# Performance work log

Measured on AMD Instinct MI355X. Metric: run time of the kernel, lower is better.

## Reference

```python
import jax, jax.numpy as jnp
import numpy as np
import math

D_MODEL = 1024
N_HEAD = 16
D_K = D_MODEL // N_HEAD
NEG_INF = -1e30  # fp32 mask fill value used by the torch module


def _rope(x, b_rotate=None):
    # x: [b, h, n, k], k even. Interleaved (even/odd) RoPE, matching the torch code.
    b, h, n, k = x.shape
    half = k // 2
    inv_freq = 1.0 / (10000.0 ** (jnp.arange(half, dtype=jnp.float32) / half))  # [half]
    ang = jnp.arange(n, dtype=jnp.float32)[:, None] * inv_freq[None, :]          # [n, half]
    sin = jnp.sin(ang)
    cos = jnp.cos(ang)
    x1 = x[..., 0::2]  # [b,h,n,half]
    x2 = x[..., 1::2]
    even = x1 * cos - x2 * sin
    odd = x1 * sin + x2 * cos
    out = jnp.stack([even, odd], axis=-1).reshape(b, h, n, k)  # re-interleave
    if b_rotate is not None:
        out = out * b_rotate  # barope multiplicative term
    return out


def setup_inputs() -> dict:
    key = jax.random.key(0)
    ks = jax.random.split(key, 7)
    B, S = 1, 2048
    query = jax.random.normal(ks[0], (B, S, D_MODEL), dtype=jnp.float32)
    kk = jax.random.normal(ks[1], (B, S, D_MODEL), dtype=jnp.float32)
    value = jax.random.normal(ks[2], (B, S, D_MODEL), dtype=jnp.float32)
    b_emb = jax.random.normal(ks[3], (B, S, D_MODEL), dtype=jnp.float32)
    mask = jax.random.bernoulli(ks[4], 0.9, (B, S))  # bool [B,S]
    linear_layers = 0.02 * jax.random.normal(ks[5], (3, D_MODEL, N_HEAD, D_K), dtype=jnp.float32)
    b_proj = jax.random.normal(ks[6], (D_MODEL, N_HEAD, D_K), dtype=jnp.float32)
    return {"query": query, "key": kk, "value": value, "b_emb": b_emb,
            "mask": mask, "linear_layers": linear_layers, "b_proj": b_proj}


def reference(query, key, value, b_emb, mask, linear_layers, b_proj):
    B, S, _ = query.shape
    # QKV projections: [b,n,d] x [d,h,k] -> [b,h,n,k]
    q = jnp.einsum('bnd,dhk->bhnk', query, linear_layers[0])
    k = jnp.einsum('bnd,dhk->bhnk', key, linear_layers[1])
    v = jnp.einsum('bnd,dhk->bhnk', value, linear_layers[2])
    # barope=True branch: multiplicative rotation modifier from b_emb
    b_rotate = jnp.einsum('bnd,dhk->bhnk', b_emb, b_proj)
    q = _rope(q, b_rotate)
    k = _rope(k, b_rotate)
    scores = jnp.einsum('bhqk,bhmk->bhqm', q, k) / math.sqrt(D_K)  # [b,h,s,s]
    pair_mask = (mask[:, :, None] & mask[:, None, :])[:, None]     # [b,1,s,s]
    scores = jnp.where(pair_mask, scores, NEG_INF)
    p_attn = jax.nn.softmax(scores, axis=-1)  # dropout p=0 -> identity
    x = jnp.einsum('bhqm,bhmk->bhqk', p_attn, v)
    return x.transpose(0, 2, 1, 3).reshape(B, S, N_HEAD * D_K)
```

## Files before the change

kernel.cpp:

```cpp
#include <hip/hip_runtime.h>
#include <hip/hip_bf16.h>
#include <math.h>

#define S_LEN 2048
#define NHEAD 16
#define DMODEL 1024

typedef short bf16x8 __attribute__((ext_vector_type(8)));
typedef float f32x4 __attribute__((ext_vector_type(4)));

static __device__ __forceinline__ unsigned short bfbits(float x) {
    __hip_bfloat16 h = __float2bfloat16(x);
    unsigned short u; __builtin_memcpy(&u, &h, 2); return u;
}
static __device__ __forceinline__ float bf2f(unsigned short u) {
    union { unsigned int i; float f; } v; v.i = ((unsigned int)u) << 16; return v.f;
}
static __device__ __forceinline__ void splitRN(float x, unsigned short& hi, unsigned short& lo) {
    unsigned short h = bfbits(x);
    float r = x - bf2f(h);
    hi = h; lo = bfbits(r);
}
static __device__ __forceinline__ void split4(float4 x, ushort4& h4, ushort4& l4) {
    unsigned short h0,l0,h1,l1,h2,l2,h3,l3;
    splitRN(x.x,h0,l0); splitRN(x.y,h1,l1); splitRN(x.z,h2,l2); splitRN(x.w,h3,l3);
    h4 = make_ushort4(h0,h1,h2,h3); l4 = make_ushort4(l0,l1,l2,l3);
}

__device__ __forceinline__ int mask_at(const void* mp, int enc, int s) {
    if (enc) return ((const unsigned char*)mp)[s] != 0;
    return ((const unsigned int*)mp)[s] != 0u;
}

__global__ void detect_kernel(const void* __restrict__ mask, int* __restrict__ flags) {
    if (threadIdx.x == 0 && blockIdx.x == 0) {
        const unsigned int* m = (const unsigned int*)mask;
        int bytey = 0;
        for (int i = 0; i < 8; ++i) {
            unsigned int u = m[i];
            if (u != 0u && u != 1u && u != 0x3F800000u) bytey = 1;
        }
        flags[0] = bytey;
    }
}

__global__ __launch_bounds__(256)
void presplit_w(const float* __restrict__ ll, const float* __restrict__ bproj,
                unsigned short* __restrict__ Wh, unsigned short* __restrict__ Wl) {
    __shared__ unsigned short Th[64][72], Tl[64][72];
    const int t = threadIdx.x;
    const int bid = blockIdx.x;
    const int stream = bid >> 8;
    const int rem = bid & 255;
    const int h = rem >> 4;
    const int d0 = (rem & 15) << 6;
    const float* src = (stream == 3) ? bproj : (ll + (size_t)stream * 1048576);
#pragma unroll
    for (int rep = 0; rep < 4; ++rep) {
        int fid = rep * 256 + t;
        int dl = fid >> 4, n4 = (fid & 15) * 4;
        float4 w = *(const float4*)&src[(size_t)(d0 + dl) * 1024 + h * 64 + n4];
        unsigned short hh, lo2;
#pragma unroll
        for (int m = 0; m < 4; ++m) { splitRN((&w.x)[m], hh, lo2); Th[n4+m][dl] = hh; Tl[n4+m][dl] = lo2; }
    }
    __syncthreads();
    size_t obase = (size_t)stream * 1048576;
#pragma unroll
    for (int rep = 0; rep < 2; ++rep) {
        int wid = rep * 256 + t;
        int n = wid >> 3, dl8 = (wid & 7) * 8;
        int dtile = n >> 4, cc = n & 15;
        int dglob = d0 + dl8;
        int kc = dglob >> 5;
        int qd = (dglob >> 3) & 3;
        size_t off = obase + (size_t)(h * 4 + dtile) * 16384 + (size_t)kc * 512
                   + (size_t)(qd * 16 + cc) * 8;
        *(uint4*)&Wh[off] = *(uint4*)&Th[n][dl8];
        *(uint4*)&Wl[off] = *(uint4*)&Tl[n][dl8];
    }
}

__global__ __launch_bounds__(256, 4)
void proj_fused5(const float* __restrict__ Xq, const float* __restrict__ Xk,
                 const float* __restrict__ Xv, const float* __restrict__ Xb,
                 const unsigned short* __restrict__ Wh, const unsigned short* __restrict__ Wl,
                 unsigned short* __restrict__ qhi, unsigned short* __restrict__ qlo,
                 unsigned short* __restrict__ khi, unsigned short* __restrict__ klo,
                 unsigned short* __restrict__ vhi) {
    __shared__ unsigned short smem[8960];
    unsigned short (*XQh)[40] = (unsigned short(*)[40])(smem + 0 * 1280);
    unsigned short (*XQl)[40] = (unsigned short(*)[40])(smem + 1 * 1280);
    unsigned short (*XKh)[40] = (unsigned short(*)[40])(smem + 2 * 1280);
    unsigned short (*XKl)[40] = (unsigned short(*)[40])(smem + 3 * 1280);
    unsigned short (*XVh)[40] = (unsigned short(*)[40])(smem + 4 * 1280);
    unsigned short (*XBh)[40] = (unsigned short(*)[40])(smem + 5 * 1280);
    unsigned short (*XBl)[40] = (unsigned short(*)[40])(smem + 6 * 1280);
    unsigned short (*T0)[72] = (unsigned short(*)[72])(smem + 0);
    unsigned short (*T1)[72] = (unsigned short(*)[72])(smem + 2304);
    unsigned short (*T2)[40] = (unsigned short(*)[40])(smem + 4608);

    const int t = threadIdx.x;
    const int lin = blockIdx.x;
    const int xcd = lin & 7;
    const int inner = lin >> 3;
    const int h = inner >> 3;
    const int sg = inner & 7;
    const int s0 = (xcd * 8 + sg) * 32;
    const int lane = t & 63, dt = t >> 6, quad = lane >> 4, c = lane & 15;

    f32x4 aq[2], ak[2], av[2], ab[2];
#pragma unroll
    for (int i = 0; i < 2; ++i) {
        aq[i] = (f32x4){0.f,0.f,0.f,0.f}; ak[i] = (f32x4){0.f,0.f,0.f,0.f};
        av[i] = (f32x4){0.f,0.f,0.f,0.f}; ab[i] = (f32x4){0.f,0.f,0.f,0.f};
    }

    const int xr = t >> 3, xc = (t & 7) * 4;
    const size_t xg = (size_t)(s0 + xr) * DMODEL + xc;
    const size_t wb = (size_t)(h * 4 + dt) * 16384 + (size_t)lane * 8;

    float4 pq, pk, pv, pb;
    pq = *(const float4*)&Xq[xg];
    pk = *(const float4*)&Xk[xg];
    pv = *(const float4*)&Xv[xg];
    pb = *(const float4*)&Xb[xg];

    for (int kc = 0; kc < 32; ++kc) {
        __syncthreads();
        {
            ushort4 h4, l4;
            split4(pq, h4, l4); *(ushort4*)&XQh[xr][xc] = h4; *(ushort4*)&XQl[xr][xc] = l4;
            split4(pk, h4, l4); *(ushort4*)&XKh[xr][xc] = h4; *(ushort4*)&XKl[xr][xc] = l4;
            split4(pb, h4, l4); *(ushort4*)&XBh[xr][xc] = h4; *(ushort4*)&XBl[xr][xc] = l4;
            *(ushort4*)&XVh[xr][xc] = make_ushort4(bfbits(pv.x),bfbits(pv.y),bfbits(pv.z),bfbits(pv.w));
        }
        __syncthreads();

        size_t wo = wb + (size_t)kc * 512;
        bf16x8 aQh = *(const bf16x8*)&Wh[wo];
        bf16x8 aQl = *(const bf16x8*)&Wl[wo];
        bf16x8 aKh = *(const bf16x8*)&Wh[1048576 + wo];
        bf16x8 aKl = *(const bf16x8*)&Wl[1048576 + wo];
        bf16x8 aVh = *(const bf16x8*)&Wh[2097152 + wo];
        bf16x8 aVl = *(const bf16x8*)&Wl[2097152 + wo];
        bf16x8 aBh = *(const bf16x8*)&Wh[3145728 + wo];
        bf16x8 aBl = *(const bf16x8*)&Wl[3145728 + wo];

        if (kc + 1 < 32) {
            size_t g = xg + (size_t)(kc + 1) * 32;
            pq = *(const float4*)&Xq[g];
            pk = *(const float4*)&Xk[g];
            pv = *(const float4*)&Xv[g];
            pb = *(const float4*)&Xb[g];
        }

#pragma unroll
        for (int st = 0; st < 2; ++st) {
            bf16x8 b1 = *(bf16x8*)&XQh[st*16+c][quad*8];
            bf16x8 b2 = *(bf16x8*)&XQl[st*16+c][quad*8];
            aq[st] = __builtin_amdgcn_mfma_f32_16x16x32_bf16(aQh, b1, aq[st], 0, 0, 0);
            aq[st] = __builtin_amdgcn_mfma_f32_16x16x32_bf16(aQh, b2, aq[st], 0, 0, 0);
            aq[st] = __builtin_amdgcn_mfma_f32_16x16x32_bf16(aQl, b1, aq[st], 0, 0, 0);
            aq[st] = __builtin_amdgcn_mfma_f32_16x16x32_bf16(aQl, b2, aq[st], 0, 0, 0);
            b1 = *(bf16x8*)&XKh[st*16+c][quad*8];
            b2 = *(bf16x8*)&XKl[st*16+c][quad*8];
            ak[st] = __builtin_amdgcn_mfma_f32_16x16x32_bf16(aKh, b1, ak[st], 0, 0, 0);
            ak[st] = __builtin_amdgcn_mfma_f32_16x16x32_bf16(aKh, b2, ak[st], 0, 0, 0);
            ak[st] = __builtin_amdgcn_mfma_f32_16x16x32_bf16(aKl, b1, ak[st], 0, 0, 0);
            ak[st] = __builtin_amdgcn_mfma_f32_16x16x32_bf16(aKl, b2, ak[st], 0, 0, 0);
            b1 = *(bf16x8*)&XVh[st*16+c][quad*8];
            av[st] = __builtin_amdgcn_mfma_f32_16x16x32_bf16(aVh, b1, av[st], 0, 0, 0);
            av[st] = __builtin_amdgcn_mfma_f32_16x16x32_bf16(aVl, b1, av[st], 0, 0, 0);
            b1 = *(bf16x8*)&XBh[st*16+c][quad*8];
            b2 = *(bf16x8*)&XBl[st*16+c][quad*8];
            ab[st] = __builtin_amdgcn_mfma_f32_16x16x32_bf16(aBh, b1, ab[st], 0, 0, 0);
            ab[st] = __builtin_amdgcn_mfma_f32_16x16x32_bf16(aBh, b2, ab[st], 0, 0, 0);
            ab[st] = __builtin_amdgcn_mfma_f32_16x16x32_bf16(aBl, b1, ab[st], 0, 0, 0);
            ab[st] = __builtin_amdgcn_mfma_f32_16x16x32_bf16(aBl, b2, ab[st], 0, 0, 0);
        }
    }

    float rq[2][4], rk[2][4];
    {
        int p0 = dt * 8 + 2 * quad;
        double inv0 = pow(10000.0, -(double)p0 / 32.0);
        double inv1 = pow(10000.0, -(double)(p0 + 1) / 32.0);
#pragma unroll
        for (int st = 0; st < 2; ++st) {
            int s = s0 + st * 16 + c;
            double a0 = (double)s * inv0, a1 = (double)s * inv1;
            float sn0 = (float)sin(a0), cs0 = (float)cos(a0);
            float sn1 = (float)sin(a1), cs1 = (float)cos(a1);
            rq[st][0] = (aq[st][0]*cs0 - aq[st][1]*sn0) * ab[st][0];
            rq[st][1] = (aq[st][0]*sn0 + aq[st][1]*cs0) * ab[st][1];
            rq[st][2] = (aq[st][2]*cs1 - aq[st][3]*sn1) * ab[st][2];
            rq[st][3] = (aq[st][2]*sn1 + aq[st][3]*cs1) * ab[st][3];
            rk[st][0] = (ak[st][0]*cs0 - ak[st][1]*sn0) * ab[st][0];
            rk[st][1] = (ak[st][0]*sn0 + ak[st][1]*cs0) * ab[st][1];
            rk[st][2] = (ak[st][2]*cs1 - ak[st][3]*sn1) * ab[st][2];
            rk[st][3] = (ak[st][2]*sn1 + ak[st][3]*cs1) * ab[st][3];
        }
    }
    __syncthreads();
#pragma unroll
    for (int st = 0; st < 2; ++st) {
        unsigned short h0,l0,h1,l1,h2,l2,h3,l3;
        splitRN(rq[st][0],h0,l0); splitRN(rq[st][1],h1,l1);
        splitRN(rq[st][2],h2,l2); splitRN(rq[st][3],h3,l3);
        *(ushort4*)&T0[st*16+c][dt*16+4*quad] = make_ushort4(h0,h1,h2,h3);
        *(ushort4*)&T1[st*16+c][dt*16+4*quad] = make_ushort4(l0,l1,l2,l3);
#pragma unroll
        for (int reg = 0; reg < 4; ++reg)
            T2[dt * 16 + 4 * quad + reg][st * 16 + c] = bfbits(av[st][reg]);
    }
    __syncthreads();
    {
        int row = t >> 3, d8 = (t & 7) * 8;
        size_t qb = ((size_t)(h * S_LEN + s0 + row)) * 64 + d8;
        *(uint4*)&qhi[qb] = *(uint4*)&T0[row][d8];
        *(uint4*)&qlo[qb] = *(uint4*)&T1[row][d8];
        int d = t >> 2, s8 = (t & 3) * 8;
        size_t vb = ((size_t)(h * 64 + d)) * S_LEN + s0 + s8;
        *(uint4*)&vhi[vb] = *(uint4*)&T2[d][s8];
    }
    __syncthreads();
#pragma unroll
    for (int st = 0; st < 2; ++st) {
        unsigned short h0,l0,h1,l1,h2,l2,h3,l3;
        splitRN(rk[st][0],h0,l0); splitRN(rk[st][1],h1,l1);
        splitRN(rk[st][2],h2,l2); splitRN(rk[st][3],h3,l3);
        *(ushort4*)&T0[st*16+c][dt*16+4*quad] = make_ushort4(h0,h1,h2,h3);
        *(ushort4*)&T1[st*16+c][dt*16+4*quad] = make_ushort4(l0,l1,l2,l3);
    }
    __syncthreads();
    {
        int row = t >> 3, d8 = (t & 7) * 8;
        size_t qb = ((size_t)(h * S_LEN + s0 + row)) * 64 + d8;
        *(uint4*)&khi[qb] = *(uint4*)&T0[row][d8];
        *(uint4*)&klo[qb] = *(uint4*)&T1[row][d8];
    }
}

__global__ __launch_bounds__(256)
void attn_mfma(const unsigned short* __restrict__ qh, const unsigned short* __restrict__ ql,
               const unsigned short* __restrict__ kh, const unsigned short* __restrict__ kl,
               const unsigned short* __restrict__ vh,
               const void* __restrict__ mask, float* __restrict__ out,
               const int* __restrict__ flags) {
    __shared__ unsigned short Kh[2][64][72], Kl[2][64][72];
    __shared__ unsigned short Vt[2][64][72];
    __shared__ unsigned short Sh[64][72], Sl[64][72];
    const int menc = flags[0];
    const int t = threadIdx.x;
    const int lin = blockIdx.x + (blockIdx.y << 5);
    const int h = (lin & 7) * 2 + ((lin >> 3) & 1);
    const int s0 = (lin >> 4) * 64;
    const int lane = t & 63, w = t >> 6, quad = lane >> 4, c = lane & 15;

    bf16x8 qfh[2], qfl[2];
#pragma unroll
    for (int ks = 0; ks < 2; ++ks) {
        size_t base = ((size_t)(h * S_LEN + s0 + 16 * w + c)) * 64 + ks * 32 + quad * 8;
        qfh[ks] = *(const bf16x8*)&qh[base];
        qfl[ks] = *(const bf16x8*)&ql[base];
    }
    int mq[4];
#pragma unroll
    for (int i = 0; i < 4; ++i) mq[i] = mask_at(mask, menc, s0 + 16 * w + quad * 4 + i);

    float m_i[4], l_i[4];
#pragma unroll
    for (int i = 0; i < 4; ++i) { m_i[i] = -INFINITY; l_i[i] = 0.0f; }
    f32x4 o_acc[4];
#pragma unroll
    for (int i = 0; i < 4; ++i) o_acc[i] = (f32x4){0.f,0.f,0.f,0.f};

    uint4 pre[6];
#pragma unroll
    for (int i = 0; i < 2; ++i) {
        int id = i * 256 + t, row = id >> 3, col8 = (id & 7) * 8;
        size_t kb = ((size_t)(h * S_LEN + row)) * 64 + col8;
        size_t vb = ((size_t)(h * 64 + row)) * S_LEN + col8;
        pre[0 + i] = *(const uint4*)&kh[kb];
        pre[2 + i] = *(const uint4*)&kl[kb];
        pre[4 + i] = *(const uint4*)&vh[vb];
    }
#pragma unroll
    for (int i = 0; i < 2; ++i) {
        int id = i * 256 + t, row = id >> 3, col8 = (id & 7) * 8;
        *(uint4*)&Kh[0][row][col8] = pre[0 + i];
        *(uint4*)&Kl[0][row][col8] = pre[2 + i];
        *(uint4*)&Vt[0][row][col8] = pre[4 + i];
    }
    __syncthreads();

    int cur = 0;
    for (int kt = 0; kt < 32; ++kt) {
        if (kt + 1 < 32) {
            const int kb0 = (kt + 1) * 64;
#pragma unroll
            for (int i = 0; i < 2; ++i) {
                int id = i * 256 + t, row = id >> 3, col8 = (id & 7) * 8;
                size_t kb = ((size_t)(h * S_LEN + kb0 + row)) * 64 + col8;
                size_t vb = ((size_t)(h * 64 + row)) * S_LEN + kb0 + col8;
                pre[0 + i] = *(const uint4*)&kh[kb];
                pre[2 + i] = *(const uint4*)&kl[kb];
                pre[4 + i] = *(const uint4*)&vh[vb];
            }
        }
        int mk[4];
#pragma unroll
        for (int nt = 0; nt < 4; ++nt) mk[nt] = mask_at(mask, menc, kt * 64 + 16 * nt + c);

        f32x4 sc[4];
#pragma unroll
        for (int i = 0; i < 4; ++i) sc[i] = (f32x4){0.f,0.f,0.f,0.f};
#pragma unroll
        for (int nt = 0; nt < 4; ++nt)
#pragma unroll
            for (int ks = 0; ks < 2; ++ks) {
                bf16x8 kfh = *(bf16x8*)&Kh[cur][nt * 16 + c][ks * 32 + quad * 8];
                bf16x8 kfl = *(bf16x8*)&Kl[cur][nt * 16 + c][ks * 32 + quad * 8];
                sc[nt] = __builtin_amdgcn_mfma_f32_16x16x32_bf16(qfh[ks], kfh, sc[nt], 0, 0, 0);
                sc[nt] = __builtin_amdgcn_mfma_f32_16x16x32_bf16(qfh[ks], kfl, sc[nt], 0, 0, 0);
                sc[nt] = __builtin_amdgcn_mfma_f32_16x16x32_bf16(qfl[ks], kfh, sc[nt], 0, 0, 0);
            }

        float sm[4][4];
#pragma unroll
        for (int nt = 0; nt < 4; ++nt)
#pragma unroll
            for (int reg = 0; reg < 4; ++reg)
                sm[nt][reg] = (mq[reg] && mk[nt]) ? sc[nt][reg] * 0.125f : -1e30f;

        float rmax[4];
#pragma unroll
        for (int reg = 0; reg < 4; ++reg)
            rmax[reg] = fmaxf(fmaxf(sm[0][reg], sm[1][reg]), fmaxf(sm[2][reg], sm[3][reg]));
#pragma unroll
        for (int off = 1; off <= 8; off <<= 1)
#pragma unroll
            for (int reg = 0; reg < 4; ++reg)
                rmax[reg] = fmaxf(rmax[reg], __shfl_xor(rmax[reg], off, 64));

        float mn[4], alpha[4];
#pragma unroll
        for (int reg = 0; reg < 4; ++reg) {
            mn[reg] = fmaxf(m_i[reg], rmax[reg]);
            alpha[reg] = __expf(m_i[reg] - mn[reg]);
            m_i[reg] = mn[reg];
        }

        float rsum[4] = {0.f, 0.f, 0.f, 0.f};
#pragma unroll
        for (int nt = 0; nt < 4; ++nt)
#pragma unroll
            for (int reg = 0; reg < 4; ++reg) {
                float e = __expf(sm[nt][reg] - mn[reg]);
                rsum[reg] += e;
                unsigned short eh, el;
                splitRN(e, eh, el);
                Sh[16 * w + quad * 4 + reg][16 * nt + c] = eh;
                Sl[16 * w + quad * 4 + reg][16 * nt + c] = el;
            }
#pragma unroll
        for (int off = 1; off <= 8; off <<= 1)
#pragma unroll
            for (int reg = 0; reg < 4; ++reg)
                rsum[reg] += __shfl_xor(rsum[reg], off, 64);
#pragma unroll
        for (int reg = 0; reg < 4; ++reg) l_i[reg] = l_i[reg] * alpha[reg] + rsum[reg];
        if (!__all(alpha[0] == 1.0f && alpha[1] == 1.0f &&
                   alpha[2] == 1.0f && alpha[3] == 1.0f)) {
#pragma unroll
            for (int nt = 0; nt < 4; ++nt)
#pragma unroll
                for (int reg = 0; reg < 4; ++reg) o_acc[nt][reg] *= alpha[reg];
        }

        if (kt + 1 < 32) {
            const int nxt = cur ^ 1;
#pragma unroll
            for (int i = 0; i < 2; ++i) {
                int id = i * 256 + t, row = id >> 3, col8 = (id & 7) * 8;
                *(uint4*)&Kh[nxt][row][col8] = pre[0 + i];
                *(uint4*)&Kl[nxt][row][col8] = pre[2 + i];
                *(uint4*)&Vt[nxt][row][col8] = pre[4 + i];
            }
        }

#pragma unroll
        for (int ks = 0; ks < 2; ++ks) {
            bf16x8 pfh = *(bf16x8*)&Sh[16 * w + c][ks * 32 + quad * 8];
            bf16x8 pfl = *(bf16x8*)&Sl[16 * w + c][ks * 32 + quad * 8];
#pragma unroll
            for (int nt = 0; nt < 4; ++nt) {
                bf16x8 vf = *(bf16x8*)&Vt[cur][nt * 16 + c][ks * 32 + quad * 8];
                o_acc[nt] = __builtin_amdgcn_mfma_f32_16x16x32_bf16(pfh, vf, o_acc[nt], 0, 0, 0);
                o_acc[nt] = __builtin_amdgcn_mfma_f32_16x16x32_bf16(pfl, vf, o_acc[nt], 0, 0, 0);
            }
        }
        __syncthreads();
        cur ^= 1;
    }

#pragma unroll
    for (int reg = 0; reg < 4; ++reg) {
        float inv = 1.0f / l_i[reg];
        int row = s0 + 16 * w + quad * 4 + reg;
#pragma unroll
        for (int nt = 0; nt < 4; ++nt)
            out[(size_t)row * 1024 + h * 64 + nt * 16 + c] = o_acc[nt][reg] * inv;
    }
}

extern "C" void kernel_launch(void* const* d_in, const int* in_sizes, int n_in,
                              void* d_out, int out_size, void* d_ws, size_t ws_size,
                              hipStream_t stream) {
    const float* query = (const float*)d_in[0];
    const float* key   = (const float*)d_in[1];
    const float* value = (const float*)d_in[2];
    const float* b_emb = (const float*)d_in[3];
    const void*  mask  = d_in[4];
    const float* ll    = (const float*)d_in[5];
    const float* bproj = (const float*)d_in[6];
    float* out = (float*)d_out;

    const size_t HSD = (size_t)NHEAD * S_LEN * 64;
    char* ws = (char*)d_ws;
    int* flags = (int*)ws;
    unsigned short* qhi = (unsigned short*)(ws + 4096);
    unsigned short* qlo = qhi + HSD;
    unsigned short* khi = qlo + HSD;
    unsigned short* klo = khi + HSD;
    unsigned short* vhi = klo + HSD;
    unsigned short* Wh  = vhi + HSD;
    unsigned short* Wl  = Wh + 4 * 1048576;

    dim3 pb(256);
    detect_kernel<<<1, 64, 0, stream>>>(mask, flags);
    presplit_w<<<1024, pb, 0, stream>>>(ll, bproj, Wh, Wl);
    proj_fused5<<<1024, pb, 0, stream>>>(query, key, value, b_emb,
                                         Wh, Wl, qhi, qlo, khi, klo, vhi);
    attn_mfma<<<dim3(32, 16), pb, 0, stream>>>(qhi, qlo, khi, klo, vhi, mask, out, flags);
}
```

Before: 268.8 us.

## Double-buffer projection LDS tiles and shrink attention blocks to two waves

The projection kernel now double-buffers its split activation tiles in LDS. It writes the next chunk while MFMAs consume the current one, which cuts the per-iteration barriers from two to one, at the cost of doubling LDS. The attention kernel moves to 128-thread blocks covering 32 query rows, giving 1024 blocks. It drops its K/V LDS double buffer in favour of register prefetch plus a single buffer with two barriers per tile. The aim is more blocks and occupancy for attention, but each block now loads K/V for fewer query rows, so global traffic per output roughly doubles.

```diff
diff --git a/kernel.cpp b/kernel.cpp
--- a/kernel.cpp
+++ b/kernel.cpp
@@ -82,20 +82,13 @@
 }
 
 __global__ __launch_bounds__(256, 4)
-void proj_fused5(const float* __restrict__ Xq, const float* __restrict__ Xk,
+void proj_fused6(const float* __restrict__ Xq, const float* __restrict__ Xk,
                  const float* __restrict__ Xv, const float* __restrict__ Xb,
                  const unsigned short* __restrict__ Wh, const unsigned short* __restrict__ Wl,
                  unsigned short* __restrict__ qhi, unsigned short* __restrict__ qlo,
                  unsigned short* __restrict__ khi, unsigned short* __restrict__ klo,
                  unsigned short* __restrict__ vhi) {
-    __shared__ unsigned short smem[8960];
-    unsigned short (*XQh)[40] = (unsigned short(*)[40])(smem + 0 * 1280);
-    unsigned short (*XQl)[40] = (unsigned short(*)[40])(smem + 1 * 1280);
-    unsigned short (*XKh)[40] = (unsigned short(*)[40])(smem + 2 * 1280);
-    unsigned short (*XKl)[40] = (unsigned short(*)[40])(smem + 3 * 1280);
-    unsigned short (*XVh)[40] = (unsigned short(*)[40])(smem + 4 * 1280);
-    unsigned short (*XBh)[40] = (unsigned short(*)[40])(smem + 5 * 1280);
-    unsigned short (*XBl)[40] = (unsigned short(*)[40])(smem + 6 * 1280);
+    __shared__ unsigned short smem[17920];
     unsigned short (*T0)[72] = (unsigned short(*)[72])(smem + 0);
     unsigned short (*T1)[72] = (unsigned short(*)[72])(smem + 2304);
     unsigned short (*T2)[40] = (unsigned short(*)[40])(smem + 4608);
@@ -120,23 +113,30 @@
     const size_t xg = (size_t)(s0 + xr) * DMODEL + xc;
     const size_t wb = (size_t)(h * 4 + dt) * 16384 + (size_t)lane * 8;
 
+#define XARR(name, b, i) unsigned short (*name)[40] = (unsigned short(*)[40])(smem + (b) * 8960 + (i) * 1280)
+
     float4 pq, pk, pv, pb;
     pq = *(const float4*)&Xq[xg];
     pk = *(const float4*)&Xk[xg];
     pv = *(const float4*)&Xv[xg];
     pb = *(const float4*)&Xb[xg];
+    {
+        XARR(XQh,0,0); XARR(XQl,0,1); XARR(XKh,0,2); XARR(XKl,0,3);
+        XARR(XVh,0,4); XARR(XBh,0,5); XARR(XBl,0,6);
+        ushort4 h4, l4;
+        split4(pq, h4, l4); *(ushort4*)&XQh[xr][xc] = h4; *(ushort4*)&XQl[xr][xc] = l4;
+        split4(pk, h4, l4); *(ushort4*)&XKh[xr][xc] = h4; *(ushort4*)&XKl[xr][xc] = l4;
+        split4(pb, h4, l4); *(ushort4*)&XBh[xr][xc] = h4; *(ushort4*)&XBl[xr][xc] = l4;
+        *(ushort4*)&XVh[xr][xc] = make_ushort4(bfbits(pv.x),bfbits(pv.y),bfbits(pv.z),bfbits(pv.w));
+    }
+    pq = *(const float4*)&Xq[xg + 32];
+    pk = *(const float4*)&Xk[xg + 32];
+    pv = *(const float4*)&Xv[xg + 32];
+    pb = *(const float4*)&Xb[xg + 32];
+    __syncthreads();
 
     for (int kc = 0; kc < 32; ++kc) {
-        __syncthreads();
-        {
-            ushort4 h4, l4;
-            split4(pq, h4, l4); *(ushort4*)&XQh[xr][xc] = h4; *(ushort4*)&XQl[xr][xc] = l4;
-            split4(pk, h4, l4); *(ushort4*)&XKh[xr][xc] = h4; *(ushort4*)&XKl[xr][xc] = l4;
-            split4(pb, h4, l4); *(ushort4*)&XBh[xr][xc] = h4; *(ushort4*)&XBl[xr][xc] = l4;
-            *(ushort4*)&XVh[xr][xc] = make_ushort4(bfbits(pv.x),bfbits(pv.y),bfbits(pv.z),bfbits(pv.w));
-        }
-        __syncthreads();
-
+        const int cb = kc & 1, nb = cb ^ 1;
         size_t wo = wb + (size_t)kc * 512;
         bf16x8 aQh = *(const bf16x8*)&Wh[wo];
         bf16x8 aQl = *(const bf16x8*)&Wl[wo];
@@ -148,38 +148,53 @@
         bf16x8 aBl = *(const bf16x8*)&Wl[3145728 + wo];
 
         if (kc + 1 < 32) {
-            size_t g = xg + (size_t)(kc + 1) * 32;
+            XARR(XQh,nb,0); XARR(XQl,nb,1); XARR(XKh,nb,2); XARR(XKl,nb,3);
+            XARR(XVh,nb,4); XARR(XBh,nb,5); XARR(XBl,nb,6);
+            ushort4 h4, l4;
+            split4(pq, h4, l4); *(ushort4*)&XQh[xr][xc] = h4; *(ushort4*)&XQl[xr][xc] = l4;
+            split4(pk, h4, l4); *(ushort4*)&XKh[xr][xc] = h4; *(ushort4*)&XKl[xr][xc] = l4;
+            split4(pb, h4, l4); *(ushort4*)&XBh[xr][xc] = h4; *(ushort4*)&XBl[xr][xc] = l4;
+            *(ushort4*)&XVh[xr][xc] = make_ushort4(bfbits(pv.x),bfbits(pv.y),bfbits(pv.z),bfbits(pv.w));
+        }
+        if (kc + 2 < 32) {
+            size_t g = xg + (size_t)(kc + 2) * 32;
             pq = *(const float4*)&Xq[g];
             pk = *(const float4*)&Xk[g];
             pv = *(const float4*)&Xv[g];
             pb = *(const float4*)&Xb[g];
         }
 
-#pragma unroll
-        for (int st = 0; st < 2; ++st) {
-            bf16x8 b1 = *(bf16x8*)&XQh[st*16+c][quad*8];
-            bf16x8 b2 = *(bf16x8*)&XQl[st*16+c][quad*8];
-            aq[st] = __builtin_amdgcn_mfma_f32_16x16x32_bf16(aQh, b1, aq[st], 0, 0, 0);
-            aq[st] = __builtin_amdgcn_mfma_f32_16x16x32_bf16(aQh, b2, aq[st], 0, 0, 0);
-            aq[st] = __builtin_amdgcn_mfma_f32_16x16x32_bf16(aQl, b1, aq[st], 0, 0, 0);
-            aq[st] = __builtin_amdgcn_mfma_f32_16x16x32_bf16(aQl, b2, aq[st], 0, 0, 0);
-            b1 = *(bf16x8*)&XKh[st*16+c][quad*8];
-            b2 = *(bf16x8*)&XKl[st*16+c][quad*8];
-            ak[st] = __builtin_amdgcn_mfma_f32_16x16x32_bf16(aKh, b1, ak[st], 0, 0, 0);
-            ak[st] = __builtin_amdgcn_mfma_f32_16x16x32_bf16(aKh, b2, ak[st], 0, 0, 0);
-            ak[st] = __builtin_amdgcn_mfma_f32_16x16x32_bf16(aKl, b1, ak[st], 0, 0, 0);
-            ak[st] = __builtin_amdgcn_mfma_f32_16x16x32_bf16(aKl, b2, ak[st], 0, 0, 0);
-            b1 = *(bf16x8*)&XVh[st*16+c][quad*8];
-            av[st] = __builtin_amdgcn_mfma_f32_16x16x32_bf16(aVh, b1, av[st], 0, 0, 0);
-            av[st] = __builtin_amdgcn_mfma_f32_16x16x32_bf16(aVl, b1, av[st], 0, 0, 0);
-            b1 = *(bf16x8*)&XBh[st*16+c][quad*8];
-            b2 = *(bf16x8*)&XBl[st*16+c][quad*8];
-            ab[st] = __builtin_amdgcn_mfma_f32_16x16x32_bf16(aBh, b1, ab[st], 0, 0, 0);
-            ab[st] = __builtin_amdgcn_mfma_f32_16x16x32_bf16(aBh, b2, ab[st], 0, 0, 0);
-            ab[st] = __builtin_amdgcn_mfma_f32_16x16x32_bf16(aBl, b1, ab[st], 0, 0, 0);
-            ab[st] = __builtin_amdgcn_mfma_f32_16x16x32_bf16(aBl, b2, ab[st], 0, 0, 0);
-        }
-    }
+        {
+            XARR(XQh,cb,0); XARR(XQl,cb,1); XARR(XKh,cb,2); XARR(XKl,cb,3);
+            XARR(XVh,cb,4); XARR(XBh,cb,5); XARR(XBl,cb,6);
+#pragma unroll
+            for (int st = 0; st < 2; ++st) {
+                bf16x8 b1 = *(bf16x8*)&XQh[st*16+c][quad*8];
+                bf16x8 b2 = *(bf16x8*)&XQl[st*16+c][quad*8];
+                aq[st] = __builtin_amdgcn_mfma_f32_16x16x32_bf16(aQh, b1, aq[st], 0, 0, 0);
+                aq[st] = __builtin_amdgcn_mfma_f32_16x16x32_bf16(aQh, b2, aq[st], 0, 0, 0);
+                aq[st] = __builtin_amdgcn_mfma_f32_16x16x32_bf16(aQl, b1, aq[st], 0, 0, 0);
+                aq[st] = __builtin_amdgcn_mfma_f32_16x16x32_bf16(aQl, b2, aq[st], 0, 0, 0);
+                b1 = *(bf16x8*)&XKh[st*16+c][quad*8];
+                b2 = *(bf16x8*)&XKl[st*16+c][quad*8];
+                ak[st] = __builtin_amdgcn_mfma_f32_16x16x32_bf16(aKh, b1, ak[st], 0, 0, 0);
+                ak[st] = __builtin_amdgcn_mfma_f32_16x16x32_bf16(aKh, b2, ak[st], 0, 0, 0);
+                ak[st] = __builtin_amdgcn_mfma_f32_16x16x32_bf16(aKl, b1, ak[st], 0, 0, 0);
+                ak[st] = __builtin_amdgcn_mfma_f32_16x16x32_bf16(aKl, b2, ak[st], 0, 0, 0);
+                b1 = *(bf16x8*)&XVh[st*16+c][quad*8];
+                av[st] = __builtin_amdgcn_mfma_f32_16x16x32_bf16(aVh, b1, av[st], 0, 0, 0);
+                av[st] = __builtin_amdgcn_mfma_f32_16x16x32_bf16(aVl, b1, av[st], 0, 0, 0);
+                b1 = *(bf16x8*)&XBh[st*16+c][quad*8];
+                b2 = *(bf16x8*)&XBl[st*16+c][quad*8];
+                ab[st] = __builtin_amdgcn_mfma_f32_16x16x32_bf16(aBh, b1, ab[st], 0, 0, 0);
+                ab[st] = __builtin_amdgcn_mfma_f32_16x16x32_bf16(aBh, b2, ab[st], 0, 0, 0);
+                ab[st] = __builtin_amdgcn_mfma_f32_16x16x32_bf16(aBl, b1, ab[st], 0, 0, 0);
+                ab[st] = __builtin_amdgcn_mfma_f32_16x16x32_bf16(aBl, b2, ab[st], 0, 0, 0);
+            }
+        }
+        __syncthreads();
+    }
+#undef XARR
 
     float rq[2][4], rk[2][4];
     {
@@ -242,20 +257,20 @@
     }
 }
 
-__global__ __launch_bounds__(256)
+__global__ __launch_bounds__(128, 2)
 void attn_mfma(const unsigned short* __restrict__ qh, const unsigned short* __restrict__ ql,
                const unsigned short* __restrict__ kh, const unsigned short* __restrict__ kl,
                const unsigned short* __restrict__ vh,
                const void* __restrict__ mask, float* __restrict__ out,
                const int* __restrict__ flags) {
-    __shared__ unsigned short Kh[2][64][72], Kl[2][64][72];
-    __shared__ unsigned short Vt[2][64][72];
-    __shared__ unsigned short Sh[64][72], Sl[64][72];
+    __shared__ unsigned short Kh[64][72], Kl[64][72];
+    __shared__ unsigned short Vt[64][72];
+    __shared__ unsigned short Sh[32][72], Sl[32][72];
     const int menc = flags[0];
     const int t = threadIdx.x;
-    const int lin = blockIdx.x + (blockIdx.y << 5);
-    const int h = (lin & 7) * 2 + ((lin >> 3) & 1);
-    const int s0 = (lin >> 4) * 64;
+    const int lin = blockIdx.x;
+    const int h = ((lin & 7) << 1) + ((lin >> 3) & 1);
+    const int s0 = (lin >> 4) * 32;
     const int lane = t & 63, w = t >> 6, quad = lane >> 4, c = lane & 15;
 
     bf16x8 qfh[2], qfl[2];
@@ -276,37 +291,38 @@
 #pragma unroll
     for (int i = 0; i < 4; ++i) o_acc[i] = (f32x4){0.f,0.f,0.f,0.f};
 
-    uint4 pre[6];
-#pragma unroll
-    for (int i = 0; i < 2; ++i) {
-        int id = i * 256 + t, row = id >> 3, col8 = (id & 7) * 8;
+    uint4 pre[12];
+#pragma unroll
+    for (int i = 0; i < 4; ++i) {
+        int id = i * 128 + t, row = id >> 3, col8 = (id & 7) * 8;
         size_t kb = ((size_t)(h * S_LEN + row)) * 64 + col8;
         size_t vb = ((size_t)(h * 64 + row)) * S_LEN + col8;
         pre[0 + i] = *(const uint4*)&kh[kb];
-        pre[2 + i] = *(const uint4*)&kl[kb];
-        pre[4 + i] = *(const uint4*)&vh[vb];
-    }
-#pragma unroll
-    for (int i = 0; i < 2; ++i) {
-        int id = i * 256 + t, row = id >> 3, col8 = (id & 7) * 8;
-        *(uint4*)&Kh[0][row][col8] = pre[0 + i];
-        *(uint4*)&Kl[0][row][col8] = pre[2 + i];
-        *(uint4*)&Vt[0][row][col8] = pre[4 + i];
-    }
-    __syncthreads();
-
-    int cur = 0;
+        pre[4 + i] = *(const uint4*)&kl[kb];
+        pre[8 + i] = *(const uint4*)&vh[vb];
+    }
+
     for (int kt = 0; kt < 32; ++kt) {
+        if (kt) __syncthreads();
+#pragma unroll
+        for (int i = 0; i < 4; ++i) {
+            int id = i * 128 + t, row = id >> 3, col8 = (id & 7) * 8;
+            *(uint4*)&Kh[row][col8] = pre[0 + i];
+            *(uint4*)&Kl[row][col8] = pre[4 + i];
+            *(uint4*)&Vt[row][col8] = pre[8 + i];
+        }
+        __syncthreads();
+
         if (kt + 1 < 32) {
             const int kb0 = (kt + 1) * 64;
 #pragma unroll
-            for (int i = 0; i < 2; ++i) {
-                int id = i * 256 + t, row = id >> 3, col8 = (id & 7) * 8;
+            for (int i = 0; i < 4; ++i) {
+                int id = i * 128 + t, row = id >> 3, col8 = (id & 7) * 8;
                 size_t kb = ((size_t)(h * S_LEN + kb0 + row)) * 64 + col8;
                 size_t vb = ((size_t)(h * 64 + row)) * S_LEN + kb0 + col8;
                 pre[0 + i] = *(const uint4*)&kh[kb];
-                pre[2 + i] = *(const uint4*)&kl[kb];
-                pre[4 + i] = *(const uint4*)&vh[vb];
+                pre[4 + i] = *(const uint4*)&kl[kb];
+                pre[8 + i] = *(const uint4*)&vh[vb];
             }
         }
         int mk[4];
@@ -320,8 +336,8 @@
         for (int nt = 0; nt < 4; ++nt)
 #pragma unroll
             for (int ks = 0; ks < 2; ++ks) {
-                bf16x8 kfh = *(bf16x8*)&Kh[cur][nt * 16 + c][ks * 32 + quad * 8];
-                bf16x8 kfl = *(bf16x8*)&Kl[cur][nt * 16 + c][ks * 32 + quad * 8];
+                bf16x8 kfh = *(bf16x8*)&Kh[nt * 16 + c][ks * 32 + quad * 8];
+                bf16x8 kfl = *(bf16x8*)&Kl[nt * 16 + c][ks * 32 + quad * 8];
                 sc[nt] = __builtin_amdgcn_mfma_f32_16x16x32_bf16(qfh[ks], kfh, sc[nt], 0, 0, 0);
                 sc[nt] = __builtin_amdgcn_mfma_f32_16x16x32_bf16(qfh[ks], kfl, sc[nt], 0, 0, 0);
                 sc[nt] = __builtin_amdgcn_mfma_f32_16x16x32_bf16(qfl[ks], kfh, sc[nt], 0, 0, 0);
@@ -379,30 +395,17 @@
                 for (int reg = 0; reg < 4; ++reg) o_acc[nt][reg] *= alpha[reg];
         }
 
-        if (kt + 1 < 32) {
-            const int nxt = cur ^ 1;
-#pragma unroll
-            for (int i = 0; i < 2; ++i) {
-                int id = i * 256 + t, row = id >> 3, col8 = (id & 7) * 8;
-                *(uint4*)&Kh[nxt][row][col8] = pre[0 + i];
-                *(uint4*)&Kl[nxt][row][col8] = pre[2 + i];
-                *(uint4*)&Vt[nxt][row][col8] = pre[4 + i];
-            }
-        }
-
 #pragma unroll
         for (int ks = 0; ks < 2; ++ks) {
             bf16x8 pfh = *(bf16x8*)&Sh[16 * w + c][ks * 32 + quad * 8];
             bf16x8 pfl = *(bf16x8*)&Sl[16 * w + c][ks * 32 + quad * 8];
 #pragma unroll
             for (int nt = 0; nt < 4; ++nt) {
-                bf16x8 vf = *(bf16x8*)&Vt[cur][nt * 16 + c][ks * 32 + quad * 8];
+                bf16x8 vf = *(bf16x8*)&Vt[nt * 16 + c][ks * 32 + quad * 8];
                 o_acc[nt] = __builtin_amdgcn_mfma_f32_16x16x32_bf16(pfh, vf, o_acc[nt], 0, 0, 0);
                 o_acc[nt] = __builtin_amdgcn_mfma_f32_16x16x32_bf16(pfl, vf, o_acc[nt], 0, 0, 0);
             }
         }
-        __syncthreads();
-        cur ^= 1;
     }
 
 #pragma unroll
@@ -438,10 +441,9 @@
     unsigned short* Wh  = vhi + HSD;
     unsigned short* Wl  = Wh + 4 * 1048576;
 
-    dim3 pb(256);
     detect_kernel<<<1, 64, 0, stream>>>(mask, flags);
-    presplit_w<<<1024, pb, 0, stream>>>(ll, bproj, Wh, Wl);
-    proj_fused5<<<1024, pb, 0, stream>>>(query, key, value, b_emb,
-                                         Wh, Wl, qhi, qlo, khi, klo, vhi);
-    attn_mfma<<<dim3(32, 16), pb, 0, stream>>>(qhi, qlo, khi, klo, vhi, mask, out, flags);
-}
+    presplit_w<<<1024, 256, 0, stream>>>(ll, bproj, Wh, Wl);
+    proj_fused6<<<1024, 256, 0, stream>>>(query, key, value, b_emb,
+                                          Wh, Wl, qhi, qlo, khi, klo, vhi);
+    attn_mfma<<<1024, 128, 0, stream>>>(qhi, qlo, khi, klo, vhi, mask, out, flags);
+}
```

Result: slower. 409.6 us (+52.4%).
